# Optimization experiments

Measured on AMD Instinct MI355X. Metric: run time of the kernel, lower is better.

The kernel has to match this reference:

```python
import jax, jax.numpy as jnp
import numpy as np

B, S, D, H = 2, 2048, 768, 12
DH = D // H  # 64

def setup_inputs() -> dict:
    key = jax.random.key(0)
    ks = jax.random.split(key, 5)
    x = jax.random.normal(ks[0], (B, S, D), dtype=jnp.float32)
    # causal mask: True = attend (lower triangular), bool -> constant w.r.t. grads
    attn_mask = jnp.tril(jnp.ones((S, S), dtype=bool))[None, None, :, :]
    c_attn_w = jax.random.normal(ks[1], (D, 3 * D), dtype=jnp.float32) * 0.02
    c_attn_b = jnp.zeros((3 * D,), dtype=jnp.float32)
    c_proj_w = jax.random.normal(ks[2], (D, D), dtype=jnp.float32) * 0.02
    c_proj_b = jnp.zeros((D,), dtype=jnp.float32)
    return {"x": x, "attn_mask": attn_mask, "c_attn_w": c_attn_w,
            "c_attn_b": c_attn_b, "c_proj_w": c_proj_w, "c_proj_b": c_proj_b}

def reference(x, attn_mask, c_attn_w, c_attn_b, c_proj_w, c_proj_b):
    # qkv projection (Conv1D == addmm)
    qkv = x @ c_attn_w + c_attn_b                      # [B,S,3D]
    q, k, v = jnp.split(qkv, 3, axis=-1)               # each [B,S,D]
    def split_heads(t):
        return t.reshape(B, S, H, DH).transpose(0, 2, 1, 3)  # [B,H,S,DH]
    q, k, v = split_heads(q), split_heads(k), split_heads(v)
    scores = jnp.einsum('bhqd,bhkd->bhqk', q, k) / jnp.sqrt(jnp.float32(DH))
    neg = jnp.asarray(-1e9, dtype=scores.dtype)
    scores = jnp.where(attn_mask, scores, neg)         # additive causal mask
    probs = jax.nn.softmax(scores, axis=-1)            # dropout: eval mode (identity)
    out = jnp.einsum('bhqk,bhkd->bhqd', probs, v)      # [B,H,S,DH]
    out = out.transpose(0, 2, 1, 3).reshape(B, S, D)   # merge heads
    return out @ c_proj_w + c_proj_b
```

## Files before the change

### kernel.cpp

```cpp
#include <hip/hip_runtime.h>
#include <cstddef>
#include <cstdint>

#define Bsz  2
#define Ssz  2048
#define Dsz  768
#define Hsz  12
#define DHsz 64
#define Msz  4096
#define N3sz 2304
#define Kdim 768

typedef short bf16x8 __attribute__((ext_vector_type(8)));
typedef short bf16x4 __attribute__((ext_vector_type(4)));
typedef float f32x4  __attribute__((ext_vector_type(4)));
typedef const __attribute__((address_space(1))) void gvoid;
typedef __attribute__((address_space(3))) void lvoid;

static __device__ __forceinline__ unsigned short f2bf(float f) {
    unsigned int u = __builtin_bit_cast(unsigned int, f);
    u += 0x7FFFu + ((u >> 16) & 1u);
    return (unsigned short)(u >> 16);
}
static __device__ __forceinline__ unsigned int pk2bf(float a, float b) {
    return (unsigned int)f2bf(a) | ((unsigned int)f2bf(b) << 16);
}

static __device__ __forceinline__ void transpose_body(
    const float* __restrict__ W, unsigned short* __restrict__ Wt, int N,
    int bx, int by, int tid, float (*T)[65])
{
    const int n0 = bx << 6;
    const int k0 = by << 6;
#pragma unroll
    for (int p = 0; p < 4; ++p) {
        const int idx = p * 256 + tid;
        const int r  = idx >> 4;
        const int c4 = (idx & 15) << 2;
        const float4 v = *(const float4*)&W[(size_t)(k0 + r) * N + n0 + c4];
        T[r][c4 + 0] = v.x; T[r][c4 + 1] = v.y;
        T[r][c4 + 2] = v.z; T[r][c4 + 3] = v.w;
    }
    __syncthreads();
#pragma unroll
    for (int p = 0; p < 4; ++p) {
        const int idx = p * 256 + tid;
        const int r  = idx >> 4;
        const int c4 = (idx & 15) << 2;
        ushort4 o;
        o.x = f2bf(T[c4 + 0][r]); o.y = f2bf(T[c4 + 1][r]);
        o.z = f2bf(T[c4 + 2][r]); o.w = f2bf(T[c4 + 3][r]);
        *(ushort4*)&Wt[(size_t)(n0 + r) * Kdim + k0 + c4] = o;
    }
}

__global__ __launch_bounds__(256) void prep_kernel(
    const float* __restrict__ X, unsigned short* __restrict__ Xb,
    const float* __restrict__ Wqkv, unsigned short* __restrict__ Wqkvt,
    const float* __restrict__ Wproj, unsigned short* __restrict__ Wprojt)
{
    __shared__ float T[64][65];
    const int bid = blockIdx.x;
    const int tid = threadIdx.x;
    if (bid < 1536) {
        const size_t i = ((size_t)bid * 256 + tid) * 8;
        const float4 a = *(const float4*)&X[i];
        const float4 b = *(const float4*)&X[i + 4];
        ushort4 lo, hi;
        lo.x = f2bf(a.x); lo.y = f2bf(a.y); lo.z = f2bf(a.z); lo.w = f2bf(a.w);
        hi.x = f2bf(b.x); hi.y = f2bf(b.y); hi.z = f2bf(b.z); hi.w = f2bf(b.w);
        *(ushort4*)&Xb[i] = lo;
        *(ushort4*)&Xb[i + 4] = hi;
    } else if (bid < 1536 + 432) {
        const int idx = bid - 1536;
        transpose_body(Wqkv, Wqkvt, N3sz, idx % 36, idx / 36, tid, T);
    } else {
        const int idx = bid - 1968;
        transpose_body(Wproj, Wprojt, Dsz, idx % 12, idx / 12, tid, T);
    }
}

template<bool QKV>
__global__ __launch_bounds__(256) void gemm_mfma_kernel(
    const unsigned short* __restrict__ A,
    const unsigned short* __restrict__ Bt,
    const float* __restrict__ bias,
    unsigned short* __restrict__ Qo, unsigned short* __restrict__ Ko,
    unsigned short* __restrict__ Vo, float* __restrict__ Out)
{
    __shared__ unsigned short Als[128 * 64];
    __shared__ unsigned short Bls[128 * 64];

    const int tid  = threadIdx.x;
    const int w    = tid >> 6;
    const int lane = tid & 63;
    const int quad = lane >> 4;
    const int t16  = lane & 15;
    const int wm   = w & 1;
    const int wn   = w >> 1;
    const int m0   = blockIdx.y << 7;
    const int n0   = blockIdx.x << 7;

    const int lrow = lane >> 3;
    const int lch  = lane & 7;
    const unsigned short* Ag = A  + (size_t)(m0 + lrow) * Kdim + ((lch ^ lrow) << 3);
    const unsigned short* Bg = Bt + (size_t)(n0 + lrow) * Kdim + ((lch ^ lrow) << 3);

    f32x4 acc[4][4];
#pragma unroll
    for (int mt = 0; mt < 4; ++mt)
#pragma unroll
        for (int nt = 0; nt < 4; ++nt) acc[mt][nt] = (f32x4)(0.f);

    for (int k0 = 0; k0 < Kdim; k0 += 64) {
        __syncthreads();
#pragma unroll
        for (int t = 0; t < 4; ++t) {
            const int i = (w << 2) + t;
            __builtin_amdgcn_global_load_lds(
                (gvoid*)(Ag + (size_t)(i << 3) * Kdim + k0),
                (lvoid*)(Als + (i << 9)), 16, 0, 0);
            __builtin_amdgcn_global_load_lds(
                (gvoid*)(Bg + (size_t)(i << 3) * Kdim + k0),
                (lvoid*)(Bls + (i << 9)), 16, 0, 0);
        }
        __syncthreads();

#pragma unroll
        for (int ks = 0; ks < 2; ++ks) {
            const int sl = (((ks << 2) + quad) ^ (t16 & 7)) << 3;
            bf16x8 af[4], bfr[4];
#pragma unroll
            for (int mt = 0; mt < 4; ++mt)
                af[mt] = *(const bf16x8*)&Als[(((wm << 6) + (mt << 4) + t16) << 6) + sl];
#pragma unroll
            for (int nt = 0; nt < 4; ++nt)
                bfr[nt] = *(const bf16x8*)&Bls[(((wn << 6) + (nt << 4) + t16) << 6) + sl];
#pragma unroll
            for (int mt = 0; mt < 4; ++mt)
#pragma unroll
                for (int nt = 0; nt < 4; ++nt)
                    acc[mt][nt] = __builtin_amdgcn_mfma_f32_16x16x32_bf16(
                        bfr[nt], af[mt], acc[mt][nt], 0, 0, 0);
        }
    }

    if (QKV) {
        const int nb  = n0 + (wn << 6);
        const int seg = nb / Dsz;
        unsigned short* dst0 = (seg == 0) ? Qo : (seg == 1) ? Ko : Vo;
        const float sc = (seg == 0) ? 0.18033688f : 1.0f;
        const int h = (nb % Dsz) >> 6;
#pragma unroll
        for (int nt = 0; nt < 4; ++nt) {
            const int n = nb + (nt << 4) + (quad << 2);
            const int d = (nt << 4) + (quad << 2);
            const float4 bn = *(const float4*)&bias[n];
#pragma unroll
            for (int mt = 0; mt < 4; ++mt) {
                const int m  = m0 + (wm << 6) + (mt << 4) + t16;
                const int bI = m >> 11;
                const int s  = m & 2047;
                uint2 o;
                o.x = pk2bf((acc[mt][nt][0] + bn.x) * sc,
                            (acc[mt][nt][1] + bn.y) * sc);
                o.y = pk2bf((acc[mt][nt][2] + bn.z) * sc,
                            (acc[mt][nt][3] + bn.w) * sc);
                *(uint2*)&dst0[(((size_t)bI * Hsz + h) * Ssz + s) * DHsz + d] = o;
            }
        }
    } else {
#pragma unroll
        for (int nt = 0; nt < 4; ++nt) {
            const int n = n0 + (wn << 6) + (nt << 4) + (quad << 2);
            const float4 bn = *(const float4*)&bias[n];
#pragma unroll
            for (int mt = 0; mt < 4; ++mt) {
                const int m = m0 + (wm << 6) + (mt << 4) + t16;
                float4 o;
                o.x = acc[mt][nt][0] + bn.x;
                o.y = acc[mt][nt][1] + bn.y;
                o.z = acc[mt][nt][2] + bn.z;
                o.w = acc[mt][nt][3] + bn.w;
                *(float4*)&Out[(size_t)m * Dsz + n] = o;
            }
        }
    }
}

__global__ __launch_bounds__(256) void attn_mfma_kernel(
    const unsigned short* __restrict__ Q, const unsigned short* __restrict__ K,
    const unsigned short* __restrict__ V, unsigned short* __restrict__ Aout)
{
    __shared__ unsigned short Kls[2][64 * 72];
    __shared__ unsigned short Vls[2][64 * 72];

    const int tid  = threadIdx.x;
    const int w    = tid >> 6;
    const int lane = tid & 63;
    const int quad = lane >> 4;
    const int t16  = lane & 15;

    const int c    = blockIdx.x & 255;
    const int slot = blockIdx.x >> 8;
    const int u    = (slot == 0) ? c : (slot == 1) ? (511 - c) : (512 + c);
    const int qt   = 31 - (u / 24);
    const int bh   = u % 24;
    const int q0   = qt << 6;
    const int bIdx = bh / Hsz;
    const int h    = bh % Hsz;

    const size_t base = (size_t)bh * Ssz * DHsz;

    const int kv_a = tid >> 3;
    const int kc_a = tid & 7;
    const int kvp  = tid & 31;
    const int dc   = tid >> 5;

    bf16x8 qf[2];
#pragma unroll
    for (int s = 0; s < 2; ++s)
        qf[s] = *(const bf16x8*)&Q[base + (size_t)(q0 + w * 16 + t16) * DHsz
                                   + s * 32 + quad * 8];

    f32x4 O[4];
    float l_ps = 0.f;
#pragma unroll
    for (int dt = 0; dt < 4; ++dt) O[dt] = (f32x4)(0.f);

    {
        const unsigned short* Kb = K + base;
        const unsigned short* Vb = V + base;
        const uint4 k0a = *(const uint4*)&Kb[(size_t)kv_a * DHsz + kc_a * 8];
        const uint4 k0b = *(const uint4*)&Kb[(size_t)(kv_a + 32) * DHsz + kc_a * 8];
        const uint4 v0a = *(const uint4*)&Vb[(size_t)(2 * kvp) * DHsz + dc * 8];
        const uint4 v0b = *(const uint4*)&Vb[(size_t)(2 * kvp + 1) * DHsz + dc * 8];
        *(uint4*)&Kls[0][kv_a * 72 + kc_a * 8] = k0a;
        *(uint4*)&Kls[0][(kv_a + 32) * 72 + kc_a * 8] = k0b;
        const unsigned short* pa = reinterpret_cast<const unsigned short*>(&v0a);
        const unsigned short* pb = reinterpret_cast<const unsigned short*>(&v0b);
#pragma unroll
        for (int j = 0; j < 8; ++j) {
            const unsigned int pk = (unsigned int)pa[j] | ((unsigned int)pb[j] << 16);
            *(unsigned int*)&Vls[0][(dc * 8 + j) * 72 + 2 * kvp] = pk;
        }
    }
    __syncthreads();

    for (int kt = 0; kt <= qt; ++kt) {
        const int cur = kt & 1;
        const int nxt = cur ^ 1;

        uint4 kr0, kr1, va, vb;
        if (kt < qt) {
            const unsigned short* Kb = K + base + (size_t)((kt + 1) << 6) * DHsz;
            const unsigned short* Vb = V + base + (size_t)((kt + 1) << 6) * DHsz;
            kr0 = *(const uint4*)&Kb[(size_t)kv_a * DHsz + kc_a * 8];
            kr1 = *(const uint4*)&Kb[(size_t)(kv_a + 32) * DHsz + kc_a * 8];
            va  = *(const uint4*)&Vb[(size_t)(2 * kvp) * DHsz + dc * 8];
            vb  = *(const uint4*)&Vb[(size_t)(2 * kvp + 1) * DHsz + dc * 8];
        }

        f32x4 St[4];
#pragma unroll
        for (int kb = 0; kb < 4; ++kb) St[kb] = (f32x4)(0.f);
#pragma unroll
        for (int s = 0; s < 2; ++s)
#pragma unroll
            for (int kb = 0; kb < 4; ++kb) {
                const bf16x8 kf = *(const bf16x8*)&Kls[cur][(kb * 16 + t16) * 72
                                                           + s * 32 + quad * 8];
                St[kb] = __builtin_amdgcn_mfma_f32_16x16x32_bf16(kf, qf[s], St[kb], 0, 0, 0);
            }

        if (kt == qt) {
            const int qrel = w * 16 + t16;
#pragma unroll
            for (int kb = 0; kb < 4; ++kb) {
                const int kvb = kb * 16 + quad * 4;
#pragma unroll
                for (int r = 0; r < 4; ++r)
                    if (kvb + r > qrel) St[kb][r] = -1e30f;
            }
        }

#pragma unroll
        for (int kb = 0; kb < 4; ++kb) {
            const float p0 = exp2f(St[kb][0]);
            const float p1 = exp2f(St[kb][1]);
            const float p2 = exp2f(St[kb][2]);
            const float p3 = exp2f(St[kb][3]);
            l_ps += (p0 + p1) + (p2 + p3);
            uint2 pk;
            pk.x = pk2bf(p0, p1);
            pk.y = pk2bf(p2, p3);
            const bf16x4 pf = __builtin_bit_cast(bf16x4, pk);
#pragma unroll
            for (int dt = 0; dt < 4; ++dt) {
                const bf16x4 vf = *(const bf16x4*)&Vls[cur][(dt * 16 + t16) * 72
                                                            + kb * 16 + quad * 4];
                O[dt] = __builtin_amdgcn_mfma_f32_16x16x16bf16_1k(vf, pf, O[dt], 0, 0, 0);
            }
        }

        if (kt < qt) {
            *(uint4*)&Kls[nxt][kv_a * 72 + kc_a * 8] = kr0;
            *(uint4*)&Kls[nxt][(kv_a + 32) * 72 + kc_a * 8] = kr1;
            const unsigned short* pa = reinterpret_cast<const unsigned short*>(&va);
            const unsigned short* pb = reinterpret_cast<const unsigned short*>(&vb);
#pragma unroll
            for (int j = 0; j < 8; ++j) {
                const unsigned int pk = (unsigned int)pa[j] | ((unsigned int)pb[j] << 16);
                *(unsigned int*)&Vls[nxt][(dc * 8 + j) * 72 + 2 * kvp] = pk;
            }
            __syncthreads();
        }
    }

    l_ps += __shfl_xor(l_ps, 16);
    l_ps += __shfl_xor(l_ps, 32);
    {
        const float inv = 1.0f / l_ps;
        const int q = q0 + w * 16 + t16;
        unsigned short* dst = Aout + ((size_t)bIdx * Ssz + q) * Dsz + (h << 6);
#pragma unroll
        for (int dt = 0; dt < 4; ++dt) {
            uint2 o;
            o.x = pk2bf(O[dt][0] * inv, O[dt][1] * inv);
            o.y = pk2bf(O[dt][2] * inv, O[dt][3] * inv);
            *(uint2*)&dst[dt * 16 + quad * 4] = o;
        }
    }
}

extern "C" void kernel_launch(void* const* d_in, const int* in_sizes, int n_in,
                              void* d_out, int out_size, void* d_ws, size_t ws_size,
                              hipStream_t stream) {
    const float* x        = (const float*)d_in[0];
    const float* c_attn_w = (const float*)d_in[2];
    const float* c_attn_b = (const float*)d_in[3];
    const float* c_proj_w = (const float*)d_in[4];
    const float* c_proj_b = (const float*)d_in[5];
    float* out = (float*)d_out;

    const size_t T = (size_t)Msz * Dsz;
    unsigned short* xb     = (unsigned short*)d_ws;
    unsigned short* Wqkvt  = xb + T;
    unsigned short* Wprojt = Wqkvt + (size_t)N3sz * Kdim;
    unsigned short* Qw     = Wprojt + (size_t)Dsz * Kdim;
    unsigned short* Kw     = Qw + T;
    unsigned short* Vw     = Kw + T;
    unsigned short* Ab     = Vw + T;

    prep_kernel<<<2112, 256, 0, stream>>>(x, xb, c_attn_w, Wqkvt, c_proj_w, Wprojt);
    gemm_mfma_kernel<true><<<dim3(N3sz / 128, Msz / 128), 256, 0, stream>>>(
        xb, Wqkvt, c_attn_b, Qw, Kw, Vw, nullptr);
    attn_mfma_kernel<<<32 * 24, 256, 0, stream>>>(Qw, Kw, Vw, Ab);
    gemm_mfma_kernel<false><<<dim3(Dsz / 128, Msz / 128), 256, 0, stream>>>(
        Ab, Wprojt, c_proj_b, nullptr, nullptr, nullptr, out);
}
```

Measured before the change: 177.6 us.

## Stage GEMM epilogues through LDS and shrink projection GEMM tiles

Splits the templated GEMM into two kernels. The QKV GEMM now stages its bf16 outputs in shared memory, then writes full 16-byte rows per head so global stores are coalesced. The projection GEMM drops from 128x128 to 64x64 tiles, raising the grid from 192 to 768 blocks to fill more CUs, and also stages its fp32 output through LDS for coalesced stores. The cost is extra syncs, more LDS in the QKV kernel, and less data reuse per block in the projection.

Result: faster. 167.9 us (-5.5%).

```diff
diff --git a/kernel.cpp b/kernel.cpp
--- a/kernel.cpp
+++ b/kernel.cpp
@@ -80,16 +80,16 @@
     }
 }
 
-template<bool QKV>
-__global__ __launch_bounds__(256) void gemm_mfma_kernel(
+__global__ __launch_bounds__(256) void qkv_gemm_kernel(
     const unsigned short* __restrict__ A,
     const unsigned short* __restrict__ Bt,
     const float* __restrict__ bias,
     unsigned short* __restrict__ Qo, unsigned short* __restrict__ Ko,
-    unsigned short* __restrict__ Vo, float* __restrict__ Out)
+    unsigned short* __restrict__ Vo)
 {
-    __shared__ unsigned short Als[128 * 64];
-    __shared__ unsigned short Bls[128 * 64];
+    __shared__ unsigned short smem[128 * 136];
+    unsigned short* Als = smem;
+    unsigned short* Bls = smem + 8192;
 
     const int tid  = threadIdx.x;
     const int w    = tid >> 6;
@@ -145,45 +145,131 @@
         }
     }
 
-    if (QKV) {
-        const int nb  = n0 + (wn << 6);
-        const int seg = nb / Dsz;
-        unsigned short* dst0 = (seg == 0) ? Qo : (seg == 1) ? Ko : Vo;
+    __syncthreads();
+    {
+        const int seg = n0 / Dsz;
         const float sc = (seg == 0) ? 0.18033688f : 1.0f;
-        const int h = (nb % Dsz) >> 6;
 #pragma unroll
         for (int nt = 0; nt < 4; ++nt) {
-            const int n = nb + (nt << 4) + (quad << 2);
-            const int d = (nt << 4) + (quad << 2);
-            const float4 bn = *(const float4*)&bias[n];
+            const int nl = (wn << 6) + (nt << 4) + (quad << 2);
+            const float4 bn = *(const float4*)&bias[n0 + nl];
 #pragma unroll
             for (int mt = 0; mt < 4; ++mt) {
-                const int m  = m0 + (wm << 6) + (mt << 4) + t16;
-                const int bI = m >> 11;
-                const int s  = m & 2047;
+                const int ml = (wm << 6) + (mt << 4) + t16;
                 uint2 o;
                 o.x = pk2bf((acc[mt][nt][0] + bn.x) * sc,
                             (acc[mt][nt][1] + bn.y) * sc);
                 o.y = pk2bf((acc[mt][nt][2] + bn.z) * sc,
                             (acc[mt][nt][3] + bn.w) * sc);
-                *(uint2*)&dst0[(((size_t)bI * Hsz + h) * Ssz + s) * DHsz + d] = o;
+                *(uint2*)&smem[ml * 136 + nl] = o;
             }
         }
-    } else {
-#pragma unroll
-        for (int nt = 0; nt < 4; ++nt) {
-            const int n = n0 + (wn << 6) + (nt << 4) + (quad << 2);
-            const float4 bn = *(const float4*)&bias[n];
-#pragma unroll
-            for (int mt = 0; mt < 4; ++mt) {
-                const int m = m0 + (wm << 6) + (mt << 4) + t16;
-                float4 o;
-                o.x = acc[mt][nt][0] + bn.x;
-                o.y = acc[mt][nt][1] + bn.y;
-                o.z = acc[mt][nt][2] + bn.z;
-                o.w = acc[mt][nt][3] + bn.w;
-                *(float4*)&Out[(size_t)m * Dsz + n] = o;
-            }
+        __syncthreads();
+        unsigned short* dst0 = (seg == 0) ? Qo : (seg == 1) ? Ko : Vo;
+        const int h0 = (n0 % Dsz) >> 6;
+        const int chunk = tid & 7;
+#pragma unroll
+        for (int p = 0; p < 8; ++p) {
+            const int unit = p * 32 + (tid >> 3);
+            const int ml = unit >> 1;
+            const int hc = unit & 1;
+            const int m  = m0 + ml;
+            const int bI = m >> 11;
+            const int s  = m & 2047;
+            const uint4 v = *(const uint4*)&smem[ml * 136 + (hc << 6) + (chunk << 3)];
+            *(uint4*)&dst0[(((size_t)bI * Hsz + h0 + hc) * Ssz + s) * DHsz
+                           + (chunk << 3)] = v;
+        }
+    }
+}
+
+__global__ __launch_bounds__(256) void proj_gemm_kernel(
+    const unsigned short* __restrict__ A,
+    const unsigned short* __restrict__ Bt,
+    const float* __restrict__ bias, float* __restrict__ Out)
+{
+    __shared__ float smemf[64 * 68];
+    unsigned short* Als = (unsigned short*)smemf;
+    unsigned short* Bls = Als + 4096;
+
+    const int tid  = threadIdx.x;
+    const int w    = tid >> 6;
+    const int lane = tid & 63;
+    const int quad = lane >> 4;
+    const int t16  = lane & 15;
+    const int wm   = w & 1;
+    const int wn   = w >> 1;
+    const int m0   = blockIdx.y << 6;
+    const int n0   = blockIdx.x << 6;
+
+    const int lrow = lane >> 3;
+    const int lch  = lane & 7;
+    const unsigned short* Ag = A  + (size_t)(m0 + lrow) * Kdim + ((lch ^ lrow) << 3);
+    const unsigned short* Bg = Bt + (size_t)(n0 + lrow) * Kdim + ((lch ^ lrow) << 3);
+
+    f32x4 acc[2][2];
+#pragma unroll
+    for (int mt = 0; mt < 2; ++mt)
+#pragma unroll
+        for (int nt = 0; nt < 2; ++nt) acc[mt][nt] = (f32x4)(0.f);
+
+    for (int k0 = 0; k0 < Kdim; k0 += 64) {
+        __syncthreads();
+#pragma unroll
+        for (int t = 0; t < 2; ++t) {
+            const int i = (w << 1) + t;
+            __builtin_amdgcn_global_load_lds(
+                (gvoid*)(Ag + (size_t)(i << 3) * Kdim + k0),
+                (lvoid*)(Als + (i << 9)), 16, 0, 0);
+            __builtin_amdgcn_global_load_lds(
+                (gvoid*)(Bg + (size_t)(i << 3) * Kdim + k0),
+                (lvoid*)(Bls + (i << 9)), 16, 0, 0);
+        }
+        __syncthreads();
+
+#pragma unroll
+        for (int ks = 0; ks < 2; ++ks) {
+            const int sl = (((ks << 2) + quad) ^ (t16 & 7)) << 3;
+            bf16x8 af[2], bfr[2];
+#pragma unroll
+            for (int mt = 0; mt < 2; ++mt)
+                af[mt] = *(const bf16x8*)&Als[(((wm << 5) + (mt << 4) + t16) << 6) + sl];
+#pragma unroll
+            for (int nt = 0; nt < 2; ++nt)
+                bfr[nt] = *(const bf16x8*)&Bls[(((wn << 5) + (nt << 4) + t16) << 6) + sl];
+#pragma unroll
+            for (int mt = 0; mt < 2; ++mt)
+#pragma unroll
+                for (int nt = 0; nt < 2; ++nt)
+                    acc[mt][nt] = __builtin_amdgcn_mfma_f32_16x16x32_bf16(
+                        bfr[nt], af[mt], acc[mt][nt], 0, 0, 0);
+        }
+    }
+
+    __syncthreads();
+#pragma unroll
+    for (int nt = 0; nt < 2; ++nt) {
+        const int nl = (wn << 5) + (nt << 4) + (quad << 2);
+        const float4 bn = *(const float4*)&bias[n0 + nl];
+#pragma unroll
+        for (int mt = 0; mt < 2; ++mt) {
+            const int ml = (wm << 5) + (mt << 4) + t16;
+            float4 o;
+            o.x = acc[mt][nt][0] + bn.x;
+            o.y = acc[mt][nt][1] + bn.y;
+            o.z = acc[mt][nt][2] + bn.z;
+            o.w = acc[mt][nt][3] + bn.w;
+            *(float4*)&smemf[ml * 68 + nl] = o;
+        }
+    }
+    __syncthreads();
+    {
+        const int c16 = tid & 15;
+#pragma unroll
+        for (int p = 0; p < 4; ++p) {
+            const int ml = p * 16 + (tid >> 4);
+            const float4 v = *(const float4*)&smemf[ml * 68 + (c16 << 2)];
+            *(float4*)&Out[(size_t)(m0 + ml) * Dsz + n0 + (c16 << 2)] = v;
         }
     }
 }
@@ -353,9 +439,9 @@
     unsigned short* Ab     = Vw + T;
 
     prep_kernel<<<2112, 256, 0, stream>>>(x, xb, c_attn_w, Wqkvt, c_proj_w, Wprojt);
-    gemm_mfma_kernel<true><<<dim3(N3sz / 128, Msz / 128), 256, 0, stream>>>(
-        xb, Wqkvt, c_attn_b, Qw, Kw, Vw, nullptr);
+    qkv_gemm_kernel<<<dim3(N3sz / 128, Msz / 128), 256, 0, stream>>>(
+        xb, Wqkvt, c_attn_b, Qw, Kw, Vw);
     attn_mfma_kernel<<<32 * 24, 256, 0, stream>>>(Qw, Kw, Vw, Ab);
-    gemm_mfma_kernel<false><<<dim3(Dsz / 128, Msz / 128), 256, 0, stream>>>(
-        Ab, Wprojt, c_proj_b, nullptr, nullptr, nullptr, out);
-}
+    proj_gemm_kernel<<<dim3(Dsz / 64, Msz / 64), 256, 0, stream>>>(
+        Ab, Wprojt, c_proj_b, out);
+}
```
